# Optimization experiments

Measured on AMD Instinct MI355X. Metric: run time of the kernel, lower is better.

## Reference

```python
import jax, jax.numpy as jnp
import numpy as np

HEADS = 4
DIM_HEAD = 32
SCALE = DIM_HEAD ** -0.5


def setup_inputs() -> dict:
    key = jax.random.key(0)
    k1, k2, k3 = jax.random.split(key, 3)
    B, C, H, W = 4, 128, 64, 64
    inner = HEADS * DIM_HEAD  # 128
    x = jax.random.normal(k1, (B, C, H, W), dtype=jnp.float32)
    # 1x1 conv weights == channel-mixing matrices [out_ch, in_ch]
    w_qkv = jax.random.normal(k2, (inner * 3, C), dtype=jnp.float32) * (C ** -0.5)
    w_proj = jax.random.normal(k3, (C, inner), dtype=jnp.float32) * (inner ** -0.5)
    b_proj = jnp.zeros((C,), dtype=jnp.float32)
    return {"x": x, "w_qkv": w_qkv, "w_proj": w_proj, "b_proj": b_proj}


def reference(x, w_qkv, w_proj, b_proj):
    b, c, h, w = x.shape
    n = h * w
    # 1x1 conv = per-pixel matmul over channels
    qkv = jnp.einsum('bchw,oc->bohw', x, w_qkv)  # [B, 3*inner, H, W]
    q, k, v = jnp.split(qkv, 3, axis=1)

    def to_heads(t):
        # [B, inner, H, W] -> [B, heads, HW, dim_head]
        return t.reshape(b, HEADS, DIM_HEAD, n).transpose(0, 1, 3, 2)

    q = to_heads(q) * SCALE
    k = to_heads(k)
    v = to_heads(v)
    # scores [B, heads, HW, HW]; softmax is max-stabilized (matches torch amax-subtract)
    scores = jnp.einsum('bhnd,bhmd->bhnm', q, k)
    attn = jax.nn.softmax(scores, axis=-1)
    out = jnp.einsum('bhnm,bhmd->bhnd', attn, v)  # [B, heads, HW, dim_head]
    out = out.transpose(0, 1, 3, 2).reshape(b, HEADS * DIM_HEAD, h, w)
    return jnp.einsum('bchw,oc->bohw', out, w_proj) + b_proj[None, :, None, None]
```

## Files before the change

### kernel.cpp

```cpp
#include <hip/hip_runtime.h>

typedef _Float16 f16;
typedef unsigned short u16;
typedef __attribute__((ext_vector_type(8))) f16 f16x8;
typedef __attribute__((ext_vector_type(4))) f16 f16x4;
typedef __attribute__((ext_vector_type(4))) float floatx4;
typedef __attribute__((ext_vector_type(2))) __fp16 h2;

union pk4 { h2 h[2]; f16x4 v; };

#define NPIX 4096
#define KT   128
#define NT   (NPIX / KT)
#define VROW 136

__global__ __launch_bounds__(256) void qkv_mfma(
    const float* __restrict__ x, const float* __restrict__ w,
    f16* __restrict__ qh, f16* __restrict__ kh, f16* __restrict__ vth)
{
    __shared__ f16 wlds[64 * 136];
    const int tid  = threadIdx.x;
    const int wave = tid >> 6;
    const int lane = tid & 63;
    const int quad = lane >> 4;
    const int l16  = lane & 15;
    const int pbase = blockIdx.x * 64;
    const int y     = blockIdx.y;
    const int b     = blockIdx.z;

#pragma unroll
    for (int i = 0; i < 8; ++i) {
        int idx = i * 256 + tid;
        int o = idx >> 5, ch = idx & 31;
        float4 wv = *(const float4*)(w + (size_t)(y * 64 + o) * 128 + ch * 4);
        f16x4 h; h[0] = (f16)wv.x; h[1] = (f16)wv.y; h[2] = (f16)wv.z; h[3] = (f16)wv.w;
        *(f16x4*)&wlds[o * 136 + ch * 4] = h;
    }
    __syncthreads();

    const float* xb = x + (size_t)b * 128 * NPIX;
    const int type = y >> 1;

    if (type < 2) {
        const int p_row = pbase + wave * 16 + l16;
        f16x8 af[4];
#pragma unroll
        for (int kc = 0; kc < 4; ++kc) {
            const int c0 = kc * 32 + quad * 8;
#pragma unroll
            for (int j = 0; j < 8; ++j)
                af[kc][j] = (f16)xb[(size_t)(c0 + j) * NPIX + p_row];
        }
        floatx4 acc[4];
#pragma unroll
        for (int n = 0; n < 4; ++n) acc[n] = floatx4{0.f, 0.f, 0.f, 0.f};
#pragma unroll
        for (int n = 0; n < 4; ++n)
#pragma unroll
            for (int kc = 0; kc < 4; ++kc) {
                f16x8 bf = *(const f16x8*)&wlds[(n * 16 + l16) * 136 + kc * 32 + quad * 8];
                acc[n] = __builtin_amdgcn_mfma_f32_16x16x32_f16(af[kc], bf, acc[n], 0, 0, 0);
            }
        const float qs = (type == 0) ? 0.17677669529663687f * 1.4426950408889634f : 1.0f;
        f16* dst = (type == 0) ? qh : kh;
#pragma unroll
        for (int n = 0; n < 4; ++n) {
            const int og   = y * 64 + n * 16 + l16;
            const int head = (og >> 5) & 3;
            const int d    = og & 31;
            f16* base = dst + (size_t)(b * 4 + head) * NPIX * 32;
#pragma unroll
            for (int r = 0; r < 4; ++r) {
                const int p = pbase + wave * 16 + quad * 4 + r;
                base[(size_t)p * 32 + d] = (f16)(acc[n][r] * qs);
            }
        }
    } else {
        const int p_col = pbase + wave * 16 + l16;
        f16x8 bf[4];
#pragma unroll
        for (int kc = 0; kc < 4; ++kc) {
            const int c0 = kc * 32 + quad * 8;
#pragma unroll
            for (int j = 0; j < 8; ++j)
                bf[kc][j] = (f16)xb[(size_t)(c0 + j) * NPIX + p_col];
        }
        floatx4 acc[4];
#pragma unroll
        for (int m = 0; m < 4; ++m) acc[m] = floatx4{0.f, 0.f, 0.f, 0.f};
#pragma unroll
        for (int m = 0; m < 4; ++m)
#pragma unroll
            for (int kc = 0; kc < 4; ++kc) {
                f16x8 af = *(const f16x8*)&wlds[(m * 16 + l16) * 136 + kc * 32 + quad * 8];
                acc[m] = __builtin_amdgcn_mfma_f32_16x16x32_f16(af, bf[kc], acc[m], 0, 0, 0);
            }
#pragma unroll
        for (int m = 0; m < 4; ++m)
#pragma unroll
            for (int r = 0; r < 4; ++r) {
                const int og   = y * 64 + m * 16 + quad * 4 + r;
                const int head = (og >> 5) & 3;
                const int d    = og & 31;
                vth[((size_t)(b * 4 + head) * 32 + d) * NPIX + p_col] = (f16)acc[m][r];
            }
    }
}

#define ATTN_STEP(BUF, KF, KFN, TNXT)                                          \
{                                                                              \
                    \
    if ((TNXT) < NT) {                                                         \
        _Pragma("unroll")                                                      \
        for (int t = 0; t < 8; ++t)                                            \
            KFN[t] = *(const f16x8*)(kp + (size_t)((TNXT) * KT + t * 16) * 32);\
    }                                                                          \
         \
    int4 nv0, nv1;                                                             \
    if ((TNXT) < NT) {                                                         \
        const int4* vs = (const int4*)(vrow + (TNXT) * KT);                    \
        nv0 = vs[vcc]; nv1 = vs[vcc + 1];                                      \
    }                                                                          \
                                        \
    f16x4 vf[8][2];                                                            \
    _Pragma("unroll")                                                          \
    for (int c = 0; c < 8; ++c) {                                              \
        _Pragma("unroll")                                                      \
        for (int dh = 0; dh < 2; ++dh)                                         \
            vf[c][dh] = *(const f16x4*)&vlds[BUF][(dh * 16 + l16) * VROW + c * 16 + quad * 4]; \
    }                                                                          \
                     \
    floatx4 st0[8], st1[8];                                                    \
    _Pragma("unroll")                                                          \
    for (int t = 0; t < 8; ++t) {                                              \
        floatx4 z = {0.f, 0.f, 0.f, 0.f};                                      \
        st0[t] = __builtin_amdgcn_mfma_f32_16x16x32_f16(KF[t], qB[0], z, 0, 0, 0); \
    }                                                                          \
    _Pragma("unroll")                                                          \
    for (int t = 0; t < 8; ++t) {                                              \
        floatx4 z = {0.f, 0.f, 0.f, 0.f};                                      \
        st1[t] = __builtin_amdgcn_mfma_f32_16x16x32_f16(KF[t], qB[1], z, 0, 0, 0); \
    }                                                                          \
           \
    f16x4 pf0[8], pf1[8];                                                      \
    float ls0 = 0.f, ls1 = 0.f;                                                \
    _Pragma("unroll")                                                          \
    for (int c = 0; c < 8; ++c) {                                              \
        float e0 = __builtin_amdgcn_exp2f(st0[c][0]);                          \
        float e1 = __builtin_amdgcn_exp2f(st0[c][1]);                          \
        float e2 = __builtin_amdgcn_exp2f(st0[c][2]);                          \
        float e3 = __builtin_amdgcn_exp2f(st0[c][3]);                          \
        pk4 u;                                                                 \
        u.h[0] = __builtin_amdgcn_cvt_pkrtz(e0, e1);                           \
        u.h[1] = __builtin_amdgcn_cvt_pkrtz(e2, e3);                           \
        pf0[c] = u.v;                                                          \
        ls0 = __builtin_amdgcn_fdot2(u.h[0], one2, ls0, false);                \
        ls0 = __builtin_amdgcn_fdot2(u.h[1], one2, ls0, false);                \
    }                                                                          \
              \
    _Pragma("unroll")                                                          \
    for (int c = 0; c < 8; ++c) {                                              \
        oacc[0][0] = __builtin_amdgcn_mfma_f32_16x16x16f16(pf0[c], vf[c][0], oacc[0][0], 0, 0, 0); \
        oacc[0][1] = __builtin_amdgcn_mfma_f32_16x16x16f16(pf0[c], vf[c][1], oacc[0][1], 0, 0, 0); \
        float e0 = __builtin_amdgcn_exp2f(st1[c][0]);                          \
        float e1 = __builtin_amdgcn_exp2f(st1[c][1]);                          \
        float e2 = __builtin_amdgcn_exp2f(st1[c][2]);                          \
        float e3 = __builtin_amdgcn_exp2f(st1[c][3]);                          \
        pk4 u;                                                                 \
        u.h[0] = __builtin_amdgcn_cvt_pkrtz(e0, e1);                           \
        u.h[1] = __builtin_amdgcn_cvt_pkrtz(e2, e3);                           \
        pf1[c] = u.v;                                                          \
        ls1 = __builtin_amdgcn_fdot2(u.h[0], one2, ls1, false);                \
        ls1 = __builtin_amdgcn_fdot2(u.h[1], one2, ls1, false);                \
    }                                                                          \
    lsum[0] += ls0; lsum[1] += ls1;                                            \
    _Pragma("unroll")                                                          \
    for (int c = 0; c < 8; ++c) {                                              \
        oacc[1][0] = __builtin_amdgcn_mfma_f32_16x16x16f16(pf1[c], vf[c][0], oacc[1][0], 0, 0, 0); \
        oacc[1][1] = __builtin_amdgcn_mfma_f32_16x16x16f16(pf1[c], vf[c][1], oacc[1][1], 0, 0, 0); \
    }                                                                          \
           \
    if ((TNXT) < NT) {                                                         \
        *(int4*)&vlds[(BUF) ^ 1][voff]     = nv0;                              \
        *(int4*)&vlds[(BUF) ^ 1][voff + 8] = nv1;                              \
    }                                                                          \
    __syncthreads();                                                           \
}

__global__ __launch_bounds__(256, 2) void attn_kernel(
    const f16* __restrict__ qh, const f16* __restrict__ kh,
    const f16* __restrict__ vth, f16* __restrict__ att)
{
    __shared__ f16 vlds[2][32 * VROW];

    const int tid  = threadIdx.x;
    const int wave = tid >> 6;
    const int lane = tid & 63;
    const int quad = lane >> 4;
    const int l16  = lane & 15;
    const int bh   = blockIdx.x;
    const int qbase = blockIdx.y * 128 + wave * 32;

    const f16* kb = kh + (size_t)bh * NPIX * 32;
    const f16* vb = vth + (size_t)bh * 32 * NPIX;
    const f16* kp = kb + (size_t)l16 * 32 + quad * 8;

    const int vr = tid >> 3, vcc = (tid & 7) * 2;
    const int voff = vr * VROW + vcc * 8;
    const f16* vrow = vb + (size_t)vr * NPIX;

    const h2 one2 = {(__fp16)1.0f, (__fp16)1.0f};

    f16x8 qB[2];
#pragma unroll
    for (int h = 0; h < 2; ++h)
        qB[h] = *(const f16x8*)(qh + ((size_t)bh * NPIX + qbase + h * 16 + l16) * 32 + quad * 8);

    floatx4 oacc[2][2];
#pragma unroll
    for (int h = 0; h < 2; ++h)
#pragma unroll
        for (int dh = 0; dh < 2; ++dh) oacc[h][dh] = floatx4{0.f, 0.f, 0.f, 0.f};
    float lsum[2] = {0.f, 0.f};

    f16x8 kfA[8], kfB[8];
    {
        const int4* vs = (const int4*)vrow;
        int4 a = vs[vcc], b2 = vs[vcc + 1];
        *(int4*)&vlds[0][voff]     = a;
        *(int4*)&vlds[0][voff + 8] = b2;
    }
#pragma unroll
    for (int t = 0; t < 8; ++t)
        kfA[t] = *(const f16x8*)(kp + (size_t)(t * 16) * 32);
    __syncthreads();

    for (int it = 0; it < NT / 2; ++it) {
        const int t0 = it * 2;
        ATTN_STEP(0, kfA, kfB, t0 + 1);
        ATTN_STEP(1, kfB, kfA, t0 + 2);
    }

#pragma unroll
    for (int h = 0; h < 2; ++h) {
        float l = lsum[h];
        l += __shfl_xor(l, 16);
        l += __shfl_xor(l, 32);
        const float inv = 1.0f / l;
#pragma unroll
        for (int r = 0; r < 4; ++r) {
            const float invr = __shfl(inv, quad * 4 + r);
            const int q = qbase + h * 16 + quad * 4 + r;
            f16* ob = att + ((size_t)bh * NPIX + q) * 32;
            ob[l16]      = (f16)(oacc[h][0][r] * invr);
            ob[16 + l16] = (f16)(oacc[h][1][r] * invr);
        }
    }
}

__global__ __launch_bounds__(256) void proj_mfma(
    const f16* __restrict__ att, const float* __restrict__ wp,
    const float* __restrict__ bp, float* __restrict__ out)
{
    __shared__ f16 wplds[128 * 136];
    __shared__ f16 alds[64 * 136];
    __shared__ float bplds[128];
    const int tid  = threadIdx.x;
    const int wave = tid >> 6;
    const int lane = tid & 63;
    const int quad = lane >> 4;
    const int l16  = lane & 15;
    const int pbase = blockIdx.x * 64;
    const int b     = blockIdx.y;

    if (tid < 128) bplds[tid] = bp[tid];
#pragma unroll
    for (int i = 0; i < 16; ++i) {
        int idx = i * 256 + tid;
        int o = idx >> 5, ch = idx & 31;
        float4 wv = *(const float4*)(wp + (size_t)o * 128 + ch * 4);
        f16x4 h; h[0] = (f16)wv.x; h[1] = (f16)wv.y; h[2] = (f16)wv.z; h[3] = (f16)wv.w;
        *(f16x4*)&wplds[o * 136 + ch * 4] = h;
    }
    const f16* ab = att + (size_t)b * 4 * NPIX * 32;
#pragma unroll
    for (int i = 0; i < 4; ++i) {
        const int p = tid >> 2, d8 = (tid & 3) * 8;
        int4 v = *(const int4*)(ab + ((size_t)i * NPIX + pbase + p) * 32 + d8);
        *(int4*)&alds[p * 136 + i * 32 + d8] = v;
    }
    __syncthreads();

    const int p_col = pbase + wave * 16 + l16;
    f16x8 bf[4];
#pragma unroll
    for (int kc = 0; kc < 4; ++kc)
        bf[kc] = *(const f16x8*)&alds[(wave * 16 + l16) * 136 + kc * 32 + quad * 8];

    floatx4 acc[8];
#pragma unroll
    for (int m = 0; m < 8; ++m) acc[m] = floatx4{0.f, 0.f, 0.f, 0.f};
#pragma unroll
    for (int m = 0; m < 8; ++m)
#pragma unroll
        for (int kc = 0; kc < 4; ++kc) {
            f16x8 af = *(const f16x8*)&wplds[(m * 16 + l16) * 136 + kc * 32 + quad * 8];
            acc[m] = __builtin_amdgcn_mfma_f32_16x16x32_f16(af, bf[kc], acc[m], 0, 0, 0);
        }

#pragma unroll
    for (int m = 0; m < 8; ++m)
#pragma unroll
        for (int r = 0; r < 4; ++r) {
            const int o = m * 16 + quad * 4 + r;
            out[((size_t)b * 128 + o) * NPIX + p_col] = acc[m][r] + bplds[o];
        }
}

extern "C" void kernel_launch(void* const* d_in, const int* in_sizes, int n_in,
                              void* d_out, int out_size, void* d_ws, size_t ws_size,
                              hipStream_t stream)
{
    const float* x      = (const float*)d_in[0];
    const float* w_qkv  = (const float*)d_in[1];
    const float* w_proj = (const float*)d_in[2];
    const float* b_proj = (const float*)d_in[3];
    float* out = (float*)d_out;

    char* ws = (char*)d_ws;
    f16* qh  = (f16*)(ws);
    f16* kh  = (f16*)(ws + (4u << 20));
    f16* vth = (f16*)(ws + (8u << 20));
    f16* att = (f16*)(ws + (12u << 20));

    qkv_mfma<<<dim3(64, 6, 4), 256, 0, stream>>>(x, w_qkv, qh, kh, vth);
    attn_kernel<<<dim3(16, 32, 1), 256, 0, stream>>>(qh, kh, vth, att);
    proj_mfma<<<dim3(64, 4, 1), 256, 0, stream>>>(att, w_proj, b_proj, out);
}
```

Measured before the change: 127.7 us.

## Split attention key range across two wave groups per block and combine via LDS

The attention kernel now launches 512-thread blocks. Waves 0-3 process the first half of the key/value tiles and waves 4-7 process the second half, each with its own double-buffered V tile in shared memory. At the end, the second group writes its partial output accumulators and row sums to LDS, and the first group adds them before normalizing and storing. This doubles the resident waves working on each query tile, to hide memory and MFMA latency better. It costs an extra LDS round-trip, a barrier, and more shared memory per block. The grid axes are also swapped, which changes block scheduling order.

Result: slower. 153.2 us (+20.0%).

```diff
diff --git a/kernel.cpp b/kernel.cpp
--- a/kernel.cpp
+++ b/kernel.cpp
@@ -11,7 +11,7 @@
 
 #define NPIX 4096
 #define KT   128
-#define NT   (NPIX / KT)
+#define NTH  16
 #define VROW 136
 
 __global__ __launch_bounds__(256) void qkv_mfma(
@@ -109,25 +109,25 @@
 
 #define ATTN_STEP(BUF, KF, KFN, TNXT)                                          \
 {                                                                              \
-                    \
-    if ((TNXT) < NT) {                                                         \
+       \
+    if ((TNXT) < NTH) {                                                        \
         _Pragma("unroll")                                                      \
         for (int t = 0; t < 8; ++t)                                            \
             KFN[t] = *(const f16x8*)(kp + (size_t)((TNXT) * KT + t * 16) * 32);\
     }                                                                          \
-         \
+          \
     int4 nv0, nv1;                                                             \
-    if ((TNXT) < NT) {                                                         \
+    if ((TNXT) < NTH) {                                                        \
         const int4* vs = (const int4*)(vrow + (TNXT) * KT);                    \
         nv0 = vs[vcc]; nv1 = vs[vcc + 1];                                      \
     }                                                                          \
-                                        \
+                             \
     f16x4 vf[8][2];                                                            \
     _Pragma("unroll")                                                          \
     for (int c = 0; c < 8; ++c) {                                              \
         _Pragma("unroll")                                                      \
         for (int dh = 0; dh < 2; ++dh)                                         \
-            vf[c][dh] = *(const f16x4*)&vlds[BUF][(dh * 16 + l16) * VROW + c * 16 + quad * 4]; \
+            vf[c][dh] = *(const f16x4*)&vlds[BUF][khalf][(dh * 16 + l16) * VROW + c * 16 + quad * 4]; \
     }                                                                          \
                      \
     floatx4 st0[8], st1[8];                                                    \
@@ -179,35 +179,39 @@
         oacc[1][0] = __builtin_amdgcn_mfma_f32_16x16x16f16(pf1[c], vf[c][0], oacc[1][0], 0, 0, 0); \
         oacc[1][1] = __builtin_amdgcn_mfma_f32_16x16x16f16(pf1[c], vf[c][1], oacc[1][1], 0, 0, 0); \
     }                                                                          \
-           \
-    if ((TNXT) < NT) {                                                         \
-        *(int4*)&vlds[(BUF) ^ 1][voff]     = nv0;                              \
-        *(int4*)&vlds[(BUF) ^ 1][voff + 8] = nv1;                              \
+          \
+    if ((TNXT) < NTH) {                                                        \
+        *(int4*)&vlds[(BUF) ^ 1][shalf][voff]     = nv0;                       \
+        *(int4*)&vlds[(BUF) ^ 1][shalf][voff + 8] = nv1;                       \
     }                                                                          \
     __syncthreads();                                                           \
 }
 
-__global__ __launch_bounds__(256, 2) void attn_kernel(
+__global__ __launch_bounds__(512, 4) void attn_kernel(
     const f16* __restrict__ qh, const f16* __restrict__ kh,
     const f16* __restrict__ vth, f16* __restrict__ att)
 {
-    __shared__ f16 vlds[2][32 * VROW];
+    __shared__ f16 vlds[2][2][32 * VROW];
 
     const int tid  = threadIdx.x;
     const int wave = tid >> 6;
     const int lane = tid & 63;
     const int quad = lane >> 4;
     const int l16  = lane & 15;
-    const int bh   = blockIdx.x;
-    const int qbase = blockIdx.y * 128 + wave * 32;
+    const int bh   = blockIdx.y;
+    const int qgrp  = wave & 3;
+    const int khalf = wave >> 2;
+    const int qbase = blockIdx.x * 128 + qgrp * 32;
 
     const f16* kb = kh + (size_t)bh * NPIX * 32;
     const f16* vb = vth + (size_t)bh * 32 * NPIX;
-    const f16* kp = kb + (size_t)l16 * 32 + quad * 8;
-
-    const int vr = tid >> 3, vcc = (tid & 7) * 2;
+    const f16* kp = kb + ((size_t)khalf * NTH * KT + l16) * 32 + quad * 8;
+
+    const int stid = tid & 255;
+    const int shalf = tid >> 8;
+    const int vr = stid >> 3, vcc = (stid & 7) * 2;
     const int voff = vr * VROW + vcc * 8;
-    const f16* vrow = vb + (size_t)vr * NPIX;
+    const f16* vrow = vb + (size_t)vr * NPIX + (size_t)shalf * NTH * KT;
 
     const h2 one2 = {(__fp16)1.0f, (__fp16)1.0f};
 
@@ -227,18 +231,47 @@
     {
         const int4* vs = (const int4*)vrow;
         int4 a = vs[vcc], b2 = vs[vcc + 1];
-        *(int4*)&vlds[0][voff]     = a;
-        *(int4*)&vlds[0][voff + 8] = b2;
+        *(int4*)&vlds[0][shalf][voff]     = a;
+        *(int4*)&vlds[0][shalf][voff + 8] = b2;
     }
 #pragma unroll
     for (int t = 0; t < 8; ++t)
         kfA[t] = *(const f16x8*)(kp + (size_t)(t * 16) * 32);
     __syncthreads();
 
-    for (int it = 0; it < NT / 2; ++it) {
+    for (int it = 0; it < NTH / 2; ++it) {
         const int t0 = it * 2;
         ATTN_STEP(0, kfA, kfB, t0 + 1);
         ATTN_STEP(1, kfB, kfA, t0 + 2);
+    }
+
+    float* comb = (float*)&vlds[0][0][0];
+    const int ci = (qgrp * 64 + lane) * 19;
+    if (khalf == 1) {
+        float* p = comb + ci;
+#pragma unroll
+        for (int h = 0; h < 2; ++h)
+#pragma unroll
+            for (int dh = 0; dh < 2; ++dh)
+#pragma unroll
+                for (int r = 0; r < 4; ++r)
+                    p[h * 8 + dh * 4 + r] = oacc[h][dh][r];
+        p[16] = lsum[0];
+        p[17] = lsum[1];
+    }
+    __syncthreads();
+    if (khalf == 1) return;
+    {
+        const float* p = comb + ci;
+#pragma unroll
+        for (int h = 0; h < 2; ++h)
+#pragma unroll
+            for (int dh = 0; dh < 2; ++dh)
+#pragma unroll
+                for (int r = 0; r < 4; ++r)
+                    oacc[h][dh][r] += p[h * 8 + dh * 4 + r];
+        lsum[0] += p[16];
+        lsum[1] += p[17];
     }
 
 #pragma unroll
@@ -334,6 +367,6 @@
     f16* att = (f16*)(ws + (12u << 20));
 
     qkv_mfma<<<dim3(64, 6, 4), 256, 0, stream>>>(x, w_qkv, qh, kh, vth);
-    attn_kernel<<<dim3(16, 32, 1), 256, 0, stream>>>(qh, kh, vth, att);
+    attn_kernel<<<dim3(32, 16, 1), 512, 0, stream>>>(qh, kh, vth, att);
     proj_mfma<<<dim3(64, 4, 1), 256, 0, stream>>>(att, w_proj, b_proj, out);
 }
```
